# Optimization experiments

Hardware: AMD Instinct MI355X
Metric: run time of the kernel (lower is better)

## Reference

```python
import jax, jax.numpy as jnp
import numpy as np

WS = 7    # window_size
SS = 3    # shift_size
NH = 12   # num_heads


def _rel_index(ws):
    # doublestepseq(2*Ww-1, Wh, 1, Ww): seq1[:,None]+seq2[None,:] -> (1, N)
    seq1 = np.arange(ws) * (2 * ws - 1)
    coords = (seq1[:, None] + np.arange(ws)[None, :]).reshape(1, -1)  # (1, N)
    rel = coords + coords.T          # (N, N)
    return np.ascontiguousarray(rel[:, ::-1])  # flip along axis 1


def _attn_mask(Hp, Wp, ws, ss):
    img = np.zeros((Hp, Wp), np.int32)
    cnt = 0
    for h in (slice(0, -ws), slice(-ws, -ss), slice(-ss, None)):
        for w in (slice(0, -ws), slice(-ws, -ss), slice(-ss, None)):
            img[h, w] = cnt
            cnt += 1
    mw = img.reshape(Hp // ws, ws, Wp // ws, ws).transpose(0, 2, 1, 3).reshape(-1, ws * ws)
    diff = mw[:, None, :] - mw[:, :, None]  # unsqueeze(1) - unsqueeze(2)
    return np.where(diff != 0, -100.0, 0.0).astype(np.float32)  # (nW, N, N)


def setup_inputs() -> dict:
    key = jax.random.key(0)
    ks = jax.random.split(key, 4)
    B, H, W, C = 8, 112, 112, 384
    x = jax.random.normal(ks[0], (B, H * W, C), jnp.float32)
    qkv_w = jax.random.normal(ks[1], (C, 3 * C), jnp.float32) * 0.02
    qkv_b = jnp.zeros((3 * C,), jnp.float32)
    proj_w = jax.random.normal(ks[2], (C, C), jnp.float32) * 0.02
    proj_b = jnp.zeros((C,), jnp.float32)
    rel_pos_table = jax.random.normal(ks[3], ((2 * WS - 1) ** 2, NH), jnp.float32) * 0.02
    return {"x": x, "qkv_w": qkv_w, "qkv_b": qkv_b, "proj_w": proj_w,
            "proj_b": proj_b, "rel_pos_table": rel_pos_table, "H": H, "W": W}


def reference(x, qkv_w, qkv_b, proj_w, proj_b, rel_pos_table, H, W):
    B, L, C = x.shape
    hd = C // NH
    scale = hd ** -0.5
    N = WS * WS
    q = x.reshape(B, H, W, C)
    pad_r = (WS - W % WS) % WS
    pad_b = (WS - H % WS) % WS
    q = jnp.pad(q, ((0, 0), (0, pad_b), (0, pad_r), (0, 0)))
    Hp, Wp = H + pad_b, W + pad_r
    # cyclic shift
    sq = jnp.roll(q, (-SS, -SS), axis=(1, 2))
    nWh, nWw = Hp // WS, Wp // WS
    nW = nWh * nWw
    # window partition -> (B*nW, N, C)
    win = sq.reshape(B, nWh, WS, nWw, WS, C).transpose(0, 1, 3, 2, 4, 5).reshape(-1, N, C)
    Bw = win.shape[0]
    qkv = (win @ qkv_w + qkv_b).reshape(Bw, N, 3, NH, hd).transpose(2, 0, 3, 1, 4)
    qh, kh, vh = qkv[0], qkv[1], qkv[2]          # (Bw, NH, N, hd)
    attn = jnp.einsum('whnd,whmd->whnm', qh * scale, kh)  # (Bw, NH, N, N)
    # relative position bias
    ridx = _rel_index(WS)
    bias = rel_pos_table[ridx.reshape(-1)].reshape(N, N, NH).transpose(2, 0, 1)
    attn = attn + bias[None]
    # shifted-window mask
    mask = jnp.asarray(_attn_mask(Hp, Wp, WS, SS))  # (nW, N, N)
    attn = attn.reshape(B, nW, NH, N, N) + mask[None, :, None]
    attn = jax.nn.softmax(attn.reshape(Bw, NH, N, N), axis=-1)
    out = jnp.einsum('whnm,whmd->whnd', attn, vh).transpose(0, 2, 1, 3).reshape(Bw, N, C)
    out = out @ proj_w + proj_b
    # window reverse + reverse shift
    sx = out.reshape(B, nWh, nWw, WS, WS, C).transpose(0, 1, 3, 2, 4, 5).reshape(B, Hp, Wp, C)
    xr = jnp.roll(sx, (SS, SS), axis=(1, 2))[:, :H, :W, :]
    return xr.reshape(B, H * W, C)
```

## Files before the change

kernel.cpp:

```cpp
#include <hip/hip_runtime.h>


typedef __bf16 bf16;
typedef __bf16 bf16x8 __attribute__((ext_vector_type(8)));
typedef float  f32x4  __attribute__((ext_vector_type(4)));

#define MFMA16(a, b, c) __builtin_amdgcn_mfma_f32_16x16x32_bf16((a), (b), (c), 0, 0, 0)

static __device__ __forceinline__ bf16x8 cvt8(const float4 lo, const float4 hi) {
    bf16x8 r;
    r[0] = (bf16)lo.x; r[1] = (bf16)lo.y; r[2] = (bf16)lo.z; r[3] = (bf16)lo.w;
    r[4] = (bf16)hi.x; r[5] = (bf16)hi.y; r[6] = (bf16)hi.z; r[7] = (bf16)hi.w;
    return r;
}

__global__ __launch_bounds__(256) void k0_prep(
    const float* __restrict__ qkv_w, const float* __restrict__ proj_w,
    const float* __restrict__ rpt,
    bf16* __restrict__ w1t, bf16* __restrict__ w2t, float* __restrict__ BT)
{
    unsigned tid = blockIdx.x * 256u + threadIdx.x;
    if (tid < 442368u) {
        unsigned n = tid / 384u, k = tid - n * 384u;
        float v = qkv_w[k * 1152u + n];
        if (n < 384u) v *= 0.17677669529663687f;
        w1t[tid] = (bf16)v;
    } else if (tid < 589824u) {
        unsigned i = tid - 442368u;
        unsigned n = i / 384u, k = i - n * 384u;
        w2t[i] = (bf16)proj_w[k * 384u + n];
    } else if (tid < 638976u) {
        unsigned i = tid - 589824u;
        unsigned h = i >> 12, r = i & 4095u, b = r >> 6, a = r & 63u;
        float v;
        if (b >= 49u) v = -1e9f;
        else if (a >= 49u) v = 0.0f;
        else {
            int ia = (int)(a / 7u), ja = (int)(a - 7u * (a / 7u));
            int ib = (int)(b / 7u), jb = (int)(b - 7u * (b / 7u));
            int ridx = 84 + 13 * (ia - ib) + (ja - jb);
            v = rpt[ridx * 12 + (int)h];
        }
        BT[i] = v;
    }
}

__global__ __launch_bounds__(256) void k1_qkv(
    const float* __restrict__ X, const bf16* __restrict__ W,
    const float* __restrict__ bias, bf16* __restrict__ Y)
{
    __shared__ __align__(16) bf16 Asm[8192];
    __shared__ __align__(16) bf16 Bsm[8192];
    unsigned id = blockIdx.x;
    unsigned xcd = id & 7u, seq = id >> 3;
    unsigned mi = seq / 9u, nblk = seq - mi * 9u;
    unsigned mblk = xcd + (mi << 3);
    unsigned tid = threadIdx.x;
    unsigned lane = tid & 63u, wv = tid >> 6;
    unsigned ln = lane & 15u, lq = lane >> 4;
    unsigned wm = wv >> 1, wn = wv & 1u;
    unsigned m0 = mblk * 128u, n0 = nblk * 128u;

    f32x4 acc[4][4] = {};

    for (unsigned kt = 0; kt < 6; ++kt) {
        unsigned k0 = kt * 64u;
        __syncthreads();
#pragma unroll
        for (unsigned r = 0; r < 8; ++r) {
            unsigned f = tid + (r << 8);
            if (f < 1024u) {
                unsigned blk = f >> 6, l = f & 63u;
                unsigned row = m0 + (blk >> 1) * 16u + (l & 15u);
                unsigned gk  = k0 + (blk & 1u) * 32u + (l >> 4) * 8u;
                const float* src = X + (size_t)row * 384u + gk;
                float4 lo = *(const float4*)src;
                float4 hi = *(const float4*)(src + 4);
                *(bf16x8*)&Asm[f * 8u] = cvt8(lo, hi);
            } else {
                unsigned g = f - 1024u;
                unsigned blk = g >> 6, l = g & 63u;
                unsigned row = n0 + (blk >> 1) * 16u + (l & 15u);
                unsigned gk  = k0 + (blk & 1u) * 32u + (l >> 4) * 8u;
                *(int4*)&Bsm[g * 8u] = *(const int4*)(W + (size_t)row * 384u + gk);
            }
        }
        __syncthreads();
#pragma unroll
        for (unsigned ks = 0; ks < 2; ++ks) {
            bf16x8 af[4], bfr[4];
#pragma unroll
            for (unsigned t = 0; t < 4; ++t)
                af[t] = *(const bf16x8*)&Asm[(((wm * 4u + t) << 1) + ks) * 512u + lane * 8u];
#pragma unroll
            for (unsigned t = 0; t < 4; ++t)
                bfr[t] = *(const bf16x8*)&Bsm[(((wn * 4u + t) << 1) + ks) * 512u + lane * 8u];
#pragma unroll
            for (unsigned i = 0; i < 4; ++i)
#pragma unroll
                for (unsigned j = 0; j < 4; ++j)
                    acc[i][j] = MFMA16(af[i], bfr[j], acc[i][j]);
        }
    }
#pragma unroll
    for (unsigned j = 0; j < 4; ++j) {
        unsigned col = n0 + wn * 64u + j * 16u + ln;
        float bv = bias[col];
        if (col < 384u) bv *= 0.17677669529663687f;
#pragma unroll
        for (unsigned i = 0; i < 4; ++i) {
            unsigned row = m0 + wm * 64u + i * 16u + lq * 4u;
#pragma unroll
            for (unsigned rg = 0; rg < 4; ++rg)
                Y[(size_t)(row + rg) * 1152u + col] = (bf16)(acc[i][j][rg] + bv);
        }
    }
}

__global__ __launch_bounds__(64) void k2_attn(
    const bf16* __restrict__ Y, const float* __restrict__ BT,
    float* __restrict__ O)
{
    __shared__ __align__(16) bf16 Pl[64 * 72];
    __shared__ __align__(16) bf16 Vt[32 * 72];
    unsigned h = blockIdx.x, bwin = blockIdx.y;
    unsigned bb = bwin >> 8, wi = bwin & 255u, wh = wi >> 4, ww = wi & 15u;
    unsigned lane = threadIdx.x, ln = lane & 15u, lq = lane >> 4;
    unsigned hw32 = h * 32u;

    auto pixrow = [&](unsigned t) -> unsigned {
        unsigned ti = t / 7u, tj = t - ti * 7u;
        unsigned gh = wh * 7u + ti + 3u; if (gh >= 112u) gh -= 112u;
        unsigned gw = ww * 7u + tj + 3u; if (gw >= 112u) gw -= 112u;
        return bb * 12544u + gh * 112u + gw;
    };

    {
        unsigned t = lane < 49u ? lane : 0u;
        const bf16* vs = Y + (size_t)pixrow(t) * 1152u + 768u + hw32;
        bf16x8 v0 = *(const bf16x8*)(vs);
        bf16x8 v1 = *(const bf16x8*)(vs + 8);
        bf16x8 v2 = *(const bf16x8*)(vs + 16);
        bf16x8 v3 = *(const bf16x8*)(vs + 24);
#pragma unroll
        for (int d = 0; d < 8; ++d) {
            Vt[(unsigned)(d     ) * 72u + lane] = v0[d];
            Vt[(unsigned)(d + 8 ) * 72u + lane] = v1[d];
            Vt[(unsigned)(d + 16) * 72u + lane] = v2[d];
            Vt[(unsigned)(d + 24) * 72u + lane] = v3[d];
        }
    }

    bf16x8 qf[4], kf[4];
#pragma unroll
    for (int i = 0; i < 4; ++i) {
        unsigned t = (unsigned)i * 16u + ln; t = t < 49u ? t : 0u;
        qf[i] = *(const bf16x8*)(Y + (size_t)pixrow(t) * 1152u + hw32 + lq * 8u);
    }
#pragma unroll
    for (int i = 0; i < 4; ++i) {
        unsigned t = (unsigned)i * 16u + ln; t = t < 49u ? t : 0u;
        kf[i] = *(const bf16x8*)(Y + (size_t)pixrow(t) * 1152u + 384u + hw32 + lq * 8u);
    }

    f32x4 s[4][4] = {};
#pragma unroll
    for (int i = 0; i < 4; ++i)
#pragma unroll
        for (int j = 0; j < 4; ++j)
            s[i][j] = MFMA16(qf[i], kf[j], s[i][j]);

    const float* bth = BT + h * 4096u;
#pragma unroll
    for (int i = 0; i < 4; ++i)
#pragma unroll
        for (int j = 0; j < 4; ++j) {
            f32x4 b = *(const f32x4*)(bth + ((unsigned)j * 16u + ln) * 64u +
                                      (unsigned)i * 16u + lq * 4u);
            s[i][j] += b;
        }

    if (wh == 15u || ww == 15u) {
        int ra[4][4], rb[4];
#pragma unroll
        for (int i = 0; i < 4; ++i)
#pragma unroll
            for (int rg = 0; rg < 4; ++rg) {
                unsigned a = (unsigned)i * 16u + lq * 4u + (unsigned)rg;
                unsigned ti = a / 7u, tj = a - ti * 7u;
                unsigned gh = wh * 7u + ti, gw = ww * 7u + tj;
                int rh = gh < 105u ? 0 : (gh < 109u ? 1 : 2);
                int rw = gw < 105u ? 0 : (gw < 109u ? 1 : 2);
                ra[i][rg] = rh * 3 + rw;
            }
#pragma unroll
        for (int j = 0; j < 4; ++j) {
            unsigned bc = (unsigned)j * 16u + ln;
            unsigned ti = bc / 7u, tj = bc - ti * 7u;
            unsigned gh = wh * 7u + ti, gw = ww * 7u + tj;
            int rh = gh < 105u ? 0 : (gh < 109u ? 1 : 2);
            int rw = gw < 105u ? 0 : (gw < 109u ? 1 : 2);
            rb[j] = rh * 3 + rw;
        }
#pragma unroll
        for (int i = 0; i < 4; ++i)
#pragma unroll
            for (int j = 0; j < 4; ++j)
#pragma unroll
                for (int rg = 0; rg < 4; ++rg)
                    if (ra[i][rg] != rb[j]) s[i][j][rg] -= 100.0f;
    }

    float rinv[4][4];
#pragma unroll
    for (int i = 0; i < 4; ++i)
#pragma unroll
        for (int rg = 0; rg < 4; ++rg) {
            float m = fmaxf(fmaxf(s[i][0][rg], s[i][1][rg]),
                            fmaxf(s[i][2][rg], s[i][3][rg]));
#pragma unroll
            for (int d = 8; d >= 1; d >>= 1) m = fmaxf(m, __shfl_xor(m, d, 64));
            float sum = 0.0f;
#pragma unroll
            for (int j = 0; j < 4; ++j) {
                float e = __expf(s[i][j][rg] - m);
                s[i][j][rg] = e;
                sum += e;
            }
#pragma unroll
            for (int d = 8; d >= 1; d >>= 1) sum += __shfl_xor(sum, d, 64);
            rinv[i][rg] = 1.0f / sum;
        }

#pragma unroll
    for (int i = 0; i < 4; ++i)
#pragma unroll
        for (int rg = 0; rg < 4; ++rg) {
            unsigned a = (unsigned)i * 16u + lq * 4u + (unsigned)rg;
#pragma unroll
            for (int j = 0; j < 4; ++j)
                Pl[a * 72u + (unsigned)j * 16u + ln] = (bf16)s[i][j][rg];
        }

    __syncthreads();

    f32x4 o[4][2] = {};
#pragma unroll
    for (int ks = 0; ks < 2; ++ks) {
        bf16x8 pf[4], vf[2];
#pragma unroll
        for (int i = 0; i < 4; ++i)
            pf[i] = *(const bf16x8*)&Pl[((unsigned)i * 16u + ln) * 72u +
                                        (unsigned)ks * 32u + lq * 8u];
#pragma unroll
        for (int c = 0; c < 2; ++c)
            vf[c] = *(const bf16x8*)&Vt[((unsigned)c * 16u + ln) * 72u +
                                        (unsigned)ks * 32u + lq * 8u];
#pragma unroll
        for (int i = 0; i < 4; ++i)
#pragma unroll
            for (int c = 0; c < 2; ++c)
                o[i][c] = MFMA16(pf[i], vf[c], o[i][c]);
    }

#pragma unroll
    for (int i = 0; i < 4; ++i)
#pragma unroll
        for (int rg = 0; rg < 4; ++rg) {
            unsigned a = (unsigned)i * 16u + lq * 4u + (unsigned)rg;
            if (a < 49u) {
                float ri = rinv[i][rg];
                size_t base = (size_t)pixrow(a) * 384u + hw32;
                O[base + ln]        = o[i][0][rg] * ri;
                O[base + 16u + ln]  = o[i][1][rg] * ri;
            }
        }
}

__global__ __launch_bounds__(768) void k3_proj(
    const float* A, const bf16* __restrict__ W,
    const float* __restrict__ bias, float* Out)
{
    __shared__ __align__(16) bf16 Asm[8192];
    __shared__ __align__(16) bf16 Bsm[24576];
    unsigned mblk = blockIdx.x;
    unsigned tid = threadIdx.x;
    unsigned lane = tid & 63u, wv = tid >> 6;
    unsigned ln = lane & 15u, lq = lane >> 4;
    unsigned wm = wv & 1u, wn = wv >> 1;
    unsigned m0 = mblk * 128u;

    f32x4 acc[4][4] = {};

    for (unsigned kt = 0; kt < 6; ++kt) {
        unsigned k0 = kt * 64u;
        __syncthreads();
        for (unsigned f = tid; f < 4096u; f += 768u) {
            if (f < 1024u) {
                unsigned blk = f >> 6, l = f & 63u;
                unsigned row = m0 + (blk >> 1) * 16u + (l & 15u);
                unsigned gk  = k0 + (blk & 1u) * 32u + (l >> 4) * 8u;
                const float* src = A + (size_t)row * 384u + gk;
                float4 lo = *(const float4*)src;
                float4 hi = *(const float4*)(src + 4);
                *(bf16x8*)&Asm[f * 8u] = cvt8(lo, hi);
            } else {
                unsigned g = f - 1024u;
                unsigned blk = g >> 6, l = g & 63u;
                unsigned row = (blk >> 1) * 16u + (l & 15u);
                unsigned gk  = k0 + (blk & 1u) * 32u + (l >> 4) * 8u;
                *(int4*)&Bsm[g * 8u] = *(const int4*)(W + (size_t)row * 384u + gk);
            }
        }
        __syncthreads();
#pragma unroll
        for (unsigned ks = 0; ks < 2; ++ks) {
            bf16x8 af[4], bfr[4];
#pragma unroll
            for (unsigned t = 0; t < 4; ++t)
                af[t] = *(const bf16x8*)&Asm[(((wm * 4u + t) << 1) + ks) * 512u + lane * 8u];
#pragma unroll
            for (unsigned t = 0; t < 4; ++t)
                bfr[t] = *(const bf16x8*)&Bsm[(((wn * 4u + t) << 1) + ks) * 512u + lane * 8u];
#pragma unroll
            for (unsigned i = 0; i < 4; ++i)
#pragma unroll
                for (unsigned j = 0; j < 4; ++j)
                    acc[i][j] = MFMA16(af[i], bfr[j], acc[i][j]);
        }
    }
#pragma unroll
    for (unsigned j = 0; j < 4; ++j) {
        unsigned col = wn * 64u + j * 16u + ln;
        float bv = bias[col];
#pragma unroll
        for (unsigned i = 0; i < 4; ++i) {
            unsigned row = m0 + wm * 64u + i * 16u + lq * 4u;
#pragma unroll
            for (unsigned rg = 0; rg < 4; ++rg)
                Out[(size_t)(row + rg) * 384u + col] = acc[i][j][rg] + bv;
        }
    }
}

extern "C" void kernel_launch(void* const* d_in, const int* in_sizes, int n_in,
                              void* d_out, int out_size, void* d_ws, size_t ws_size,
                              hipStream_t stream) {
    const float* x      = (const float*)d_in[0];
    const float* qkv_w  = (const float*)d_in[1];
    const float* qkv_b  = (const float*)d_in[2];
    const float* proj_w = (const float*)d_in[3];
    const float* proj_b = (const float*)d_in[4];
    const float* rpt    = (const float*)d_in[5];
    (void)in_sizes; (void)n_in; (void)out_size; (void)ws_size;

    char* ws = (char*)d_ws;
    bf16*  Y   = (bf16*)(ws);
    bf16*  w1t = (bf16*)(ws + 231211008u);
    bf16*  w2t = (bf16*)(ws + 232095744u);
    float* BT  = (float*)(ws + 232390656u);
    float* out = (float*)d_out;

    k0_prep<<<2496, 256, 0, stream>>>(qkv_w, proj_w, rpt, w1t, w2t, BT);
    k1_qkv<<<7056, 256, 0, stream>>>(x, w1t, qkv_b, Y);
    k2_attn<<<dim3(12, 2048), 64, 0, stream>>>(Y, BT, out);
    k3_proj<<<784, 768, 0, stream>>>(out, w2t, proj_b, out);
}
```

Measured before the change: 813.9 us.

## Keep weight tile resident in LDS, stream A from global, store attention output as bf16

Both GEMMs now preload a whole 64-column slice of the bf16 weight (all K) into LDS once per block. Each wave reads its 64x384 A rows straight from global memory into MFMA fragments, which removes the per-K-tile LDS staging and the barriers around it. The attention kernel writes its output as bf16 into the unused Q slot of Y instead of fp32 to a separate buffer, so the projection GEMM reads half the bytes and skips a conversion. The cost is a different block tiling (256x64 tiles, more blocks, occupancy hint of 3), direct uncoalesced global A fragment loads, and reduced precision of the intermediate.

```diff
diff --git a/kernel.cpp b/kernel.cpp
--- a/kernel.cpp
+++ b/kernel.cpp
@@ -45,71 +45,57 @@
     }
 }
 
-__global__ __launch_bounds__(256) void k1_qkv(
+__global__ __launch_bounds__(256, 3) void k1_qkv(
     const float* __restrict__ X, const bf16* __restrict__ W,
     const float* __restrict__ bias, bf16* __restrict__ Y)
 {
-    __shared__ __align__(16) bf16 Asm[8192];
-    __shared__ __align__(16) bf16 Bsm[8192];
+    __shared__ __align__(16) bf16 Bs[24576];
     unsigned id = blockIdx.x;
     unsigned xcd = id & 7u, seq = id >> 3;
-    unsigned mi = seq / 9u, nblk = seq - mi * 9u;
+    unsigned mi = seq / 18u, nb = seq - mi * 18u;
     unsigned mblk = xcd + (mi << 3);
     unsigned tid = threadIdx.x;
     unsigned lane = tid & 63u, wv = tid >> 6;
     unsigned ln = lane & 15u, lq = lane >> 4;
-    unsigned wm = wv >> 1, wn = wv & 1u;
-    unsigned m0 = mblk * 128u, n0 = nblk * 128u;
+    unsigned m0 = mblk * 256u, n0 = nb * 64u;
+
+    for (unsigned c = tid; c < 3072u; c += 256u) {
+        unsigned row = c / 48u, kc = c - row * 48u, k = kc * 8u;
+        unsigned blk = (k >> 5) * 4u + (row >> 4);
+        unsigned l = (row & 15u) | ((kc & 3u) << 4);
+        *(int4*)&Bs[(blk * 64u + l) * 8u] = *(const int4*)(W + (size_t)(n0 + row) * 384u + k);
+    }
+    __syncthreads();
 
     f32x4 acc[4][4] = {};
-
-    for (unsigned kt = 0; kt < 6; ++kt) {
-        unsigned k0 = kt * 64u;
-        __syncthreads();
-#pragma unroll
-        for (unsigned r = 0; r < 8; ++r) {
-            unsigned f = tid + (r << 8);
-            if (f < 1024u) {
-                unsigned blk = f >> 6, l = f & 63u;
-                unsigned row = m0 + (blk >> 1) * 16u + (l & 15u);
-                unsigned gk  = k0 + (blk & 1u) * 32u + (l >> 4) * 8u;
-                const float* src = X + (size_t)row * 384u + gk;
-                float4 lo = *(const float4*)src;
-                float4 hi = *(const float4*)(src + 4);
-                *(bf16x8*)&Asm[f * 8u] = cvt8(lo, hi);
-            } else {
-                unsigned g = f - 1024u;
-                unsigned blk = g >> 6, l = g & 63u;
-                unsigned row = n0 + (blk >> 1) * 16u + (l & 15u);
-                unsigned gk  = k0 + (blk & 1u) * 32u + (l >> 4) * 8u;
-                *(int4*)&Bsm[g * 8u] = *(const int4*)(W + (size_t)row * 384u + gk);
-            }
-        }
-        __syncthreads();
-#pragma unroll
-        for (unsigned ks = 0; ks < 2; ++ks) {
-            bf16x8 af[4], bfr[4];
-#pragma unroll
-            for (unsigned t = 0; t < 4; ++t)
-                af[t] = *(const bf16x8*)&Asm[(((wm * 4u + t) << 1) + ks) * 512u + lane * 8u];
-#pragma unroll
-            for (unsigned t = 0; t < 4; ++t)
-                bfr[t] = *(const bf16x8*)&Bsm[(((wn * 4u + t) << 1) + ks) * 512u + lane * 8u];
-#pragma unroll
-            for (unsigned i = 0; i < 4; ++i)
-#pragma unroll
-                for (unsigned j = 0; j < 4; ++j)
-                    acc[i][j] = MFMA16(af[i], bfr[j], acc[i][j]);
-        }
-    }
+    unsigned rbase = m0 + wv * 64u;
+
+#pragma unroll
+    for (unsigned kt = 0; kt < 12; ++kt) {
+        bf16x8 af[4], bfr[4];
+#pragma unroll
+        for (unsigned i = 0; i < 4; ++i) {
+            const float* p = X + (size_t)(rbase + i * 16u + ln) * 384u + kt * 32u + lq * 8u;
+            af[i] = cvt8(*(const float4*)p, *(const float4*)(p + 4));
+        }
+#pragma unroll
+        for (unsigned j = 0; j < 4; ++j)
+            bfr[j] = *(const bf16x8*)&Bs[((kt * 4u + j) * 64u + lane) * 8u];
+#pragma unroll
+        for (unsigned i = 0; i < 4; ++i)
+#pragma unroll
+            for (unsigned j = 0; j < 4; ++j)
+                acc[i][j] = MFMA16(af[i], bfr[j], acc[i][j]);
+    }
+
 #pragma unroll
     for (unsigned j = 0; j < 4; ++j) {
-        unsigned col = n0 + wn * 64u + j * 16u + ln;
+        unsigned col = n0 + j * 16u + ln;
         float bv = bias[col];
         if (col < 384u) bv *= 0.17677669529663687f;
 #pragma unroll
         for (unsigned i = 0; i < 4; ++i) {
-            unsigned row = m0 + wm * 64u + i * 16u + lq * 4u;
+            unsigned row = rbase + i * 16u + lq * 4u;
 #pragma unroll
             for (unsigned rg = 0; rg < 4; ++rg)
                 Y[(size_t)(row + rg) * 1152u + col] = (bf16)(acc[i][j][rg] + bv);
@@ -118,8 +104,7 @@
 }
 
 __global__ __launch_bounds__(64) void k2_attn(
-    const bf16* __restrict__ Y, const float* __restrict__ BT,
-    float* __restrict__ O)
+    bf16* __restrict__ Y, const float* __restrict__ BT)
 {
     __shared__ __align__(16) bf16 Pl[64 * 72];
     __shared__ __align__(16) bf16 Vt[32 * 72];
@@ -270,72 +255,62 @@
             unsigned a = (unsigned)i * 16u + lq * 4u + (unsigned)rg;
             if (a < 49u) {
                 float ri = rinv[i][rg];
-                size_t base = (size_t)pixrow(a) * 384u + hw32;
-                O[base + ln]        = o[i][0][rg] * ri;
-                O[base + 16u + ln]  = o[i][1][rg] * ri;
+                size_t base = (size_t)pixrow(a) * 1152u + hw32;
+                Y[base + ln]       = (bf16)(o[i][0][rg] * ri);
+                Y[base + 16u + ln] = (bf16)(o[i][1][rg] * ri);
             }
         }
 }
 
-__global__ __launch_bounds__(768) void k3_proj(
-    const float* A, const bf16* __restrict__ W,
-    const float* __restrict__ bias, float* Out)
+__global__ __launch_bounds__(256, 3) void k3_proj(
+    const bf16* __restrict__ A, const bf16* __restrict__ W,
+    const float* __restrict__ bias, float* __restrict__ Out)
 {
-    __shared__ __align__(16) bf16 Asm[8192];
-    __shared__ __align__(16) bf16 Bsm[24576];
-    unsigned mblk = blockIdx.x;
+    __shared__ __align__(16) bf16 Bs[24576];
+    unsigned id = blockIdx.x;
+    unsigned xcd = id & 7u, seq = id >> 3;
+    unsigned mi = seq / 6u, nb = seq - mi * 6u;
+    unsigned mblk = xcd + (mi << 3);
     unsigned tid = threadIdx.x;
     unsigned lane = tid & 63u, wv = tid >> 6;
     unsigned ln = lane & 15u, lq = lane >> 4;
-    unsigned wm = wv & 1u, wn = wv >> 1;
-    unsigned m0 = mblk * 128u;
+    unsigned m0 = mblk * 256u, n0 = nb * 64u;
+
+    for (unsigned c = tid; c < 3072u; c += 256u) {
+        unsigned row = c / 48u, kc = c - row * 48u, k = kc * 8u;
+        unsigned blk = (k >> 5) * 4u + (row >> 4);
+        unsigned l = (row & 15u) | ((kc & 3u) << 4);
+        *(int4*)&Bs[(blk * 64u + l) * 8u] = *(const int4*)(W + (size_t)(n0 + row) * 384u + k);
+    }
+    __syncthreads();
 
     f32x4 acc[4][4] = {};
-
-    for (unsigned kt = 0; kt < 6; ++kt) {
-        unsigned k0 = kt * 64u;
-        __syncthreads();
-        for (unsigned f = tid; f < 4096u; f += 768u) {
-            if (f < 1024u) {
-                unsigned blk = f >> 6, l = f & 63u;
-                unsigned row = m0 + (blk >> 1) * 16u + (l & 15u);
-                unsigned gk  = k0 + (blk & 1u) * 32u + (l >> 4) * 8u;
-                const float* src = A + (size_t)row * 384u + gk;
-                float4 lo = *(const float4*)src;
-                float4 hi = *(const float4*)(src + 4);
-                *(bf16x8*)&Asm[f * 8u] = cvt8(lo, hi);
-            } else {
-                unsigned g = f - 1024u;
-                unsigned blk = g >> 6, l = g & 63u;
-                unsigned row = (blk >> 1) * 16u + (l & 15u);
-                unsigned gk  = k0 + (blk & 1u) * 32u + (l >> 4) * 8u;
-                *(int4*)&Bsm[g * 8u] = *(const int4*)(W + (size_t)row * 384u + gk);
-            }
-        }
-        __syncthreads();
-#pragma unroll
-        for (unsigned ks = 0; ks < 2; ++ks) {
-            bf16x8 af[4], bfr[4];
-#pragma unroll
-            for (unsigned t = 0; t < 4; ++t)
-                af[t] = *(const bf16x8*)&Asm[(((wm * 4u + t) << 1) + ks) * 512u + lane * 8u];
-#pragma unroll
-            for (unsigned t = 0; t < 4; ++t)
-                bfr[t] = *(const bf16x8*)&Bsm[(((wn * 4u + t) << 1) + ks) * 512u + lane * 8u];
-#pragma unroll
-            for (unsigned i = 0; i < 4; ++i)
-#pragma unroll
-                for (unsigned j = 0; j < 4; ++j)
-                    acc[i][j] = MFMA16(af[i], bfr[j], acc[i][j]);
-        }
-    }
+    unsigned rbase = m0 + wv * 64u;
+
+#pragma unroll
+    for (unsigned kt = 0; kt < 12; ++kt) {
+        bf16x8 af[4], bfr[4];
+#pragma unroll
+        for (unsigned i = 0; i < 4; ++i)
+            af[i] = *(const bf16x8*)(A + (size_t)(rbase + i * 16u + ln) * 1152u +
+                                     kt * 32u + lq * 8u);
+#pragma unroll
+        for (unsigned j = 0; j < 4; ++j)
+            bfr[j] = *(const bf16x8*)&Bs[((kt * 4u + j) * 64u + lane) * 8u];
+#pragma unroll
+        for (unsigned i = 0; i < 4; ++i)
+#pragma unroll
+            for (unsigned j = 0; j < 4; ++j)
+                acc[i][j] = MFMA16(af[i], bfr[j], acc[i][j]);
+    }
+
 #pragma unroll
     for (unsigned j = 0; j < 4; ++j) {
-        unsigned col = wn * 64u + j * 16u + ln;
+        unsigned col = n0 + j * 16u + ln;
         float bv = bias[col];
 #pragma unroll
         for (unsigned i = 0; i < 4; ++i) {
-            unsigned row = m0 + wm * 64u + i * 16u + lq * 4u;
+            unsigned row = rbase + i * 16u + lq * 4u;
 #pragma unroll
             for (unsigned rg = 0; rg < 4; ++rg)
                 Out[(size_t)(row + rg) * 384u + col] = acc[i][j][rg] + bv;
@@ -363,6 +338,6 @@
 
     k0_prep<<<2496, 256, 0, stream>>>(qkv_w, proj_w, rpt, w1t, w2t, BT);
     k1_qkv<<<7056, 256, 0, stream>>>(x, w1t, qkv_b, Y);
-    k2_attn<<<dim3(12, 2048), 64, 0, stream>>>(Y, BT, out);
-    k3_proj<<<784, 768, 0, stream>>>(out, w2t, proj_b, out);
-}
+    k2_attn<<<dim3(12, 2048), 64, 0, stream>>>(Y, BT);
+    k3_proj<<<2352, 256, 0, stream>>>(Y, w2t, proj_b, out);
+}
```

After: 790.2 us. -2.9%, faster.
